# Optimization experiments

Measured on AMD Instinct MI355X. Metric: run time of the kernel, lower is better.

Reference implementation:

```python
import jax, jax.numpy as jnp
import numpy as np

B, T, C, H = 8, 2048, 1024, 128

def setup_inputs() -> dict:
    key = jax.random.key(0)
    kx, kq, kk, kv = jax.random.split(key, 4)
    x = jax.random.normal(kx, (B, T, C), dtype=jnp.float32)
    Wq = jax.random.normal(kq, (C, H), dtype=jnp.float32) * 0.02
    Wk = jax.random.normal(kk, (C, H), dtype=jnp.float32) * 0.02
    Wv = jax.random.normal(kv, (C, H), dtype=jnp.float32) * 0.02
    return {"x": x, "Wq": Wq, "Wk": Wk, "Wv": Wv}

def reference(x, Wq, Wk, Wv):
    # q,k,v: [B,T,H] via bias-free dense projections
    q = jnp.einsum('btc,ch->bth', x, Wq)
    k = jnp.einsum('btc,ch->bth', x, Wk)
    v = jnp.einsum('btc,ch->bth', x, Wv)
    scale = k.shape[-1] ** (-0.5)
    # scores: [B,T,T]
    wei = jnp.einsum('bth,bsh->bts', q, k) * scale
    Tlen = x.shape[1]
    causal = jnp.tril(jnp.ones((Tlen, Tlen), dtype=bool))  # True = keep
    wei = jnp.where(causal[None, :, :], wei, -jnp.inf)
    wei = jax.nn.softmax(wei, axis=-1)
    return jnp.einsum('bts,bsh->bth', wei, v)
```

## Files before the change

kernel.cpp:

```cpp
#include <hip/hip_runtime.h>

#define B_ 8
#define T_ 2048
#define C_ 1024
#define H_ 128
#define BT_ (B_*T_)

typedef unsigned short u16;
typedef unsigned int u32;
typedef __attribute__((ext_vector_type(4))) float f32x4;
typedef __attribute__((ext_vector_type(8))) __bf16 bf16x8;

__device__ __forceinline__ u16 f2bf(float f) {
  u32 u = __float_as_uint(f);
  u += 0x7fffu + ((u >> 16) & 1u);
  return (u16)(u >> 16);
}

#define GLL16(g, l) __builtin_amdgcn_global_load_lds( \
    (const __attribute__((address_space(1))) void*)(g), \
    (__attribute__((address_space(3))) void*)(l), 16, 0, 0)

__device__ __forceinline__ bf16x8 load_frag(const u16* base, int stride, int row0, int k0, int lane) {
  const u16* p = base + (size_t)(row0 + (lane & 15)) * stride + k0 + ((lane >> 4) << 3);
  return *reinterpret_cast<const bf16x8*>(p);
}

__device__ __forceinline__ bf16x8 cvt8(f32x4 lo, f32x4 hi) {
  union { u16 h[8]; bf16x8 v; } u;
#pragma unroll
  for (int i = 0; i < 4; i++) { u.h[i] = f2bf(lo[i]); u.h[4 + i] = f2bf(hi[i]); }
  return u.v;
}

__global__ void wt_kernel(const float* __restrict__ Wq, const float* __restrict__ Wk,
                          const float* __restrict__ Wv, u16* __restrict__ wt) {
  int mat = blockIdx.y;
  const float* W = (mat == 0) ? Wq : (mat == 1) ? Wk : Wv;
  int i = blockIdx.x * 256 + threadIdx.x;
  int h = i >> 10;
  int c = i & 1023;
  wt[mat * (C_ * H_) + i] = f2bf(W[c * H_ + h]);
}

__global__ __launch_bounds__(512) void qkv_gemm(const float* __restrict__ x, const u16* __restrict__ wt,
                                                u16* __restrict__ q, u16* __restrict__ k2,
                                                u16* __restrict__ vt) {
  __shared__ __align__(16) float As[2][64 * 32];
  __shared__ __align__(16) u16 Bs[2][3 * 128 * 32];
  int t = threadIdx.x;
  int lane = t & 63, w = t >> 6;
  int wm = w >> 2, wn = w & 3;
  int quad = lane >> 4, col = lane & 15;
  int m0 = blockIdx.x * 64;

  int arow = t >> 3;
  int agr = (t & 7) ^ (arow & 7);
  const float* axg = x + (size_t)(m0 + arow) * C_ + agr * 4;
  const u16* bwg = wt + (size_t)(t >> 2) * C_ + (t & 3) * 8;

  GLL16(axg, &As[0][w * 256]);
#pragma unroll
  for (int p = 0; p < 3; p++)
    GLL16(bwg + (size_t)p * 128 * C_, &Bs[0][p * 4096 + w * 512]);

  f32x4 acc[2][6] = {};
  for (int kk = 0; kk < 32; kk++) {
    int cur = kk & 1, nxt = cur ^ 1;
    __syncthreads();
    if (kk + 1 < 32) {
      int kn = (kk + 1) * 32;
      GLL16(axg + kn, &As[nxt][w * 256]);
#pragma unroll
      for (int p = 0; p < 3; p++)
        GLL16(bwg + (size_t)p * 128 * C_ + kn, &Bs[nxt][p * 4096 + w * 512]);
    }
    const float* Ab = &As[cur][0];
    const u16* Bb = &Bs[cur][0];
    bf16x8 af[2];
#pragma unroll
    for (int mt = 0; mt < 2; mt++) {
      int r = wm * 32 + mt * 16 + col;
      int s0 = (quad * 2) ^ (r & 7);
      int s1 = (quad * 2 + 1) ^ (r & 7);
      f32x4 lo = *reinterpret_cast<const f32x4*>(Ab + r * 32 + s0 * 4);
      f32x4 hi = *reinterpret_cast<const f32x4*>(Ab + r * 32 + s1 * 4);
      af[mt] = cvt8(lo, hi);
    }
    bf16x8 bfr[6];
#pragma unroll
    for (int nt = 0; nt < 6; nt++) {
      int n = wn * 96 + nt * 16 + col;
      bfr[nt] = *reinterpret_cast<const bf16x8*>(Bb + n * 32 + quad * 8);
    }
#pragma unroll
    for (int mt = 0; mt < 2; mt++)
#pragma unroll
      for (int nt = 0; nt < 6; nt++)
        acc[mt][nt] = __builtin_amdgcn_mfma_f32_16x16x32_bf16(af[mt], bfr[nt], acc[mt][nt], 0, 0, 0);
  }

#pragma unroll
  for (int mt = 0; mt < 2; mt++) {
    int row0 = m0 + wm * 32 + mt * 16 + quad * 4;
#pragma unroll
    for (int nt = 0; nt < 6; nt++) {
      int n = wn * 96 + nt * 16 + col;
      int mat = n >> 7, h = n & 127;
      if (mat == 0) {
#pragma unroll
        for (int r = 0; r < 4; r++) q[(size_t)(row0 + r) * H_ + h] = f2bf(acc[mt][nt][r]);
      } else if (mat == 1) {
#pragma unroll
        for (int r = 0; r < 4; r++) k2[(size_t)(row0 + r) * H_ + h] = f2bf(acc[mt][nt][r]);
      } else {
        int bb = row0 >> 11, tt = row0 & 2047;
        ushort4 pk;
        pk.x = f2bf(acc[mt][nt][0]); pk.y = f2bf(acc[mt][nt][1]);
        pk.z = f2bf(acc[mt][nt][2]); pk.w = f2bf(acc[mt][nt][3]);
        *reinterpret_cast<ushort4*>(&vt[((size_t)bb * H_ + h) * T_ + tt]) = pk;
      }
    }
  }
}

__global__ __launch_bounds__(256) void attn_part(const u16* __restrict__ q, const u16* __restrict__ k,
                                                 const u16* __restrict__ vt,
                                                 float* __restrict__ Op, float* __restrict__ lsum) {
  __shared__ __align__(16) u16 Ks[2][32 * 136];
  __shared__ __align__(16) u16 Vs[2][128 * 40];
  __shared__ __align__(16) u16 P[4][2][16 * 40];
  int t = threadIdx.x;
  int lane = t & 63, w = t >> 6;
  int quad = lane >> 4, col = lane & 15;
  int bx = blockIdx.x;
  int qt = 31 - (bx >> 4);
  int s = (bx >> 3) & 1;
  int b = bx & 7;
  const float scale = 0.08838834764831845f;

  int nk = 2 * (qt + 1);
  int n0 = qt + 1;
  int it0 = s ? n0 : 0;
  int it1 = s ? nk : n0;

  int krow0 = t >> 4, ke = (t & 15) * 8;
  int krow1 = krow0 + 16;
  int vrow0 = t >> 2, ve = (t & 3) * 8;
  int vrow1 = vrow0 + 64;

  int qrow0 = b * T_ + qt * 64 + w * 16;
  bf16x8 qf[4];
#pragma unroll
  for (int ks = 0; ks < 4; ks++) qf[ks] = load_frag(q, H_, qrow0, ks * 32, lane);

  f32x4 o[8] = {};
  float l[4] = {0.f, 0.f, 0.f, 0.f};
  int myqrow = qt * 64 + w * 16 + quad * 4;

  {
    const u16* kb = k + (size_t)(b * T_ + it0 * 32) * H_;
    *reinterpret_cast<uint4*>(&Ks[0][krow0 * 136 + ke]) = *reinterpret_cast<const uint4*>(kb + (size_t)krow0 * 128 + ke);
    *reinterpret_cast<uint4*>(&Ks[0][krow1 * 136 + ke]) = *reinterpret_cast<const uint4*>(kb + (size_t)krow1 * 128 + ke);
    const u16* vb = vt + (size_t)b * H_ * T_ + it0 * 32;
    *reinterpret_cast<uint4*>(&Vs[0][vrow0 * 40 + ve]) = *reinterpret_cast<const uint4*>(vb + (size_t)vrow0 * T_ + ve);
    *reinterpret_cast<uint4*>(&Vs[0][vrow1 * 40 + ve]) = *reinterpret_cast<const uint4*>(vb + (size_t)vrow1 * T_ + ve);
  }

  for (int kt = it0; kt < it1; kt++) {
    int cur = (kt - it0) & 1;
    __syncthreads();
    bool more = (kt + 1 < it1);
    uint4 kc0, kc1, vc0, vc1;
    if (more) {
      const u16* kb = k + (size_t)(b * T_ + (kt + 1) * 32) * H_;
      kc0 = *reinterpret_cast<const uint4*>(kb + (size_t)krow0 * 128 + ke);
      kc1 = *reinterpret_cast<const uint4*>(kb + (size_t)krow1 * 128 + ke);
      const u16* vb = vt + (size_t)b * H_ * T_ + (kt + 1) * 32;
      vc0 = *reinterpret_cast<const uint4*>(vb + (size_t)vrow0 * T_ + ve);
      vc1 = *reinterpret_cast<const uint4*>(vb + (size_t)vrow1 * T_ + ve);
    }

    f32x4 s0 = {}, s1 = {};
#pragma unroll
    for (int ks = 0; ks < 4; ks++) {
      bf16x8 kb0 = *reinterpret_cast<const bf16x8*>(&Ks[cur][col * 136 + ks * 32 + quad * 8]);
      bf16x8 kb1 = *reinterpret_cast<const bf16x8*>(&Ks[cur][(col + 16) * 136 + ks * 32 + quad * 8]);
      s0 = __builtin_amdgcn_mfma_f32_16x16x32_bf16(qf[ks], kb0, s0, 0, 0, 0);
      s1 = __builtin_amdgcn_mfma_f32_16x16x32_bf16(qf[ks], kb1, s1, 0, 0, 0);
    }

    float pv[8];
    int kcol0 = kt * 32 + col;
#pragma unroll
    for (int r = 0; r < 4; r++) {
      int qr = myqrow + r;
      float a0 = fminf(s0[r] * scale, 30.f);
      float a1 = fminf(s1[r] * scale, 30.f);
      a0 = (kcol0      > qr) ? -1e30f : a0;
      a1 = (kcol0 + 16 > qr) ? -1e30f : a1;
      float p0 = __expf(a0);
      float p1 = __expf(a1);
      pv[r] = p0; pv[4 + r] = p1;
      l[r] += p0 + p1;
    }

    u16* Pb = &P[w][cur][0];
#pragma unroll
    for (int r = 0; r < 4; r++) {
      Pb[(quad * 4 + r) * 40 + col] = f2bf(pv[r]);
      Pb[(quad * 4 + r) * 40 + col + 16] = f2bf(pv[4 + r]);
    }
    asm volatile("" ::: "memory");
    __builtin_amdgcn_s_waitcnt(0xc07f);
    asm volatile("" ::: "memory");
    bf16x8 pf = *reinterpret_cast<const bf16x8*>(&Pb[col * 40 + (quad << 3)]);

#pragma unroll
    for (int ht = 0; ht < 8; ht++) {
      bf16x8 vf = *reinterpret_cast<const bf16x8*>(&Vs[cur][(ht * 16 + col) * 40 + quad * 8]);
      o[ht] = __builtin_amdgcn_mfma_f32_16x16x32_bf16(pf, vf, o[ht], 0, 0, 0);
    }

    if (more) {
      int nxt = cur ^ 1;
      *reinterpret_cast<uint4*>(&Ks[nxt][krow0 * 136 + ke]) = kc0;
      *reinterpret_cast<uint4*>(&Ks[nxt][krow1 * 136 + ke]) = kc1;
      *reinterpret_cast<uint4*>(&Vs[nxt][vrow0 * 40 + ve]) = vc0;
      *reinterpret_cast<uint4*>(&Vs[nxt][vrow1 * 40 + ve]) = vc1;
    }
  }

#pragma unroll
  for (int r = 0; r < 4; r++) {
    float v = l[r];
    v += __shfl_xor(v, 1);
    v += __shfl_xor(v, 2);
    v += __shfl_xor(v, 4);
    v += __shfl_xor(v, 8);
    l[r] = v;
  }

  int tile = (s * 8 + b) * 32 + qt;
  float* Orow = Op + (size_t)tile * (64 * 128);
  float* lrow = lsum + (size_t)tile * 64;
  int rowin0 = w * 16 + quad * 4;
  if (col == 0) {
#pragma unroll
    for (int r = 0; r < 4; r++) lrow[rowin0 + r] = l[r];
  }
#pragma unroll
  for (int ht = 0; ht < 8; ht++) {
#pragma unroll
    for (int r = 0; r < 4; r++)
      Orow[(size_t)(rowin0 + r) * 128 + ht * 16 + col] = o[ht][r];
  }
}

__global__ __launch_bounds__(256) void attn_comb(const float* __restrict__ Op, const float* __restrict__ lsum,
                                                 float* __restrict__ out) {
  int bx = blockIdx.x;
  int b = bx >> 5, qt = bx & 31;
  int t = threadIdx.x;
  int h = t & 127, half = t >> 7;
  int tile0 = b * 32 + qt;
  int tile1 = tile0 + 256;
#pragma unroll 4
  for (int rr = 0; rr < 32; rr++) {
    int row = half * 32 + rr;
    float l0 = lsum[tile0 * 64 + row];
    float l1 = lsum[tile1 * 64 + row];
    float rl = 1.f / (l0 + l1);
    float v = (Op[(size_t)tile0 * 8192 + row * 128 + h] +
               Op[(size_t)tile1 * 8192 + row * 128 + h]) * rl;
    out[((size_t)(b * T_ + qt * 64 + row)) * H_ + h] = v;
  }
}

extern "C" void kernel_launch(void* const* d_in, const int* in_sizes, int n_in,
                              void* d_out, int out_size, void* d_ws, size_t ws_size,
                              hipStream_t stream) {
  (void)in_sizes; (void)n_in; (void)out_size; (void)ws_size;
  const float* x  = (const float*)d_in[0];
  const float* Wq = (const float*)d_in[1];
  const float* Wk = (const float*)d_in[2];
  const float* Wv = (const float*)d_in[3];
  u16* ws = (u16*)d_ws;
  u16* q  = ws;
  u16* k  = ws + (size_t)BT_ * H_;
  u16* vt = ws + 2 * (size_t)BT_ * H_;
  u16* wt = ws + 3 * (size_t)BT_ * H_;
  float* Op = (float*)(ws + 3 * (size_t)BT_ * H_ + 3 * C_ * H_);
  float* lsum = Op + (size_t)512 * 64 * 128;
  float* out = (float*)d_out;

  wt_kernel<<<dim3(512, 3), 256, 0, stream>>>(Wq, Wk, Wv, wt);
  qkv_gemm<<<dim3(256), 512, 0, stream>>>(x, wt, q, k, vt);
  attn_part<<<dim3(512), 256, 0, stream>>>(q, k, vt, Op, lsum);
  attn_comb<<<dim3(256), 256, 0, stream>>>(Op, lsum, out);
}
```

Baseline: 180.9 us.

## Split QKV projection GEMM across a grid dimension per weight matrix

The fused QKV GEMM, which computed all three projections per 64-row tile with 512 threads, becomes one block per (row tile, matrix) with 256 threads and a 64x128 output tile. This triples the block count from 256 to 768 so all compute units have work, and shrinks shared memory per block. In exchange, each x tile is loaded from global memory and converted to bf16 three times instead of once.

```diff
diff --git a/kernel.cpp b/kernel.cpp
--- a/kernel.cpp
+++ b/kernel.cpp
@@ -43,37 +43,41 @@
   wt[mat * (C_ * H_) + i] = f2bf(W[c * H_ + h]);
 }
 
-__global__ __launch_bounds__(512) void qkv_gemm(const float* __restrict__ x, const u16* __restrict__ wt,
+__global__ __launch_bounds__(256) void qkv_gemm(const float* __restrict__ x, const u16* __restrict__ wt,
                                                 u16* __restrict__ q, u16* __restrict__ k2,
                                                 u16* __restrict__ vt) {
   __shared__ __align__(16) float As[2][64 * 32];
-  __shared__ __align__(16) u16 Bs[2][3 * 128 * 32];
+  __shared__ __align__(16) u16 Bs[2][128 * 32];
   int t = threadIdx.x;
   int lane = t & 63, w = t >> 6;
-  int wm = w >> 2, wn = w & 3;
+  int wm = w >> 1, wn = w & 1;
   int quad = lane >> 4, col = lane & 15;
   int m0 = blockIdx.x * 64;
-
-  int arow = t >> 3;
-  int agr = (t & 7) ^ (arow & 7);
-  const float* axg = x + (size_t)(m0 + arow) * C_ + agr * 4;
-  const u16* bwg = wt + (size_t)(t >> 2) * C_ + (t & 3) * 8;
-
-  GLL16(axg, &As[0][w * 256]);
-#pragma unroll
-  for (int p = 0; p < 3; p++)
-    GLL16(bwg + (size_t)p * 128 * C_, &Bs[0][p * 4096 + w * 512]);
-
-  f32x4 acc[2][6] = {};
+  int mat = blockIdx.y;
+  const u16* wmp = wt + (size_t)mat * (C_ * H_);
+
+  int ar0 = t >> 3, ar1 = ar0 + 32;
+  const float* ax0 = x + (size_t)(m0 + ar0) * C_ + (((t & 7) ^ (ar0 & 7)) << 2);
+  const float* ax1 = x + (size_t)(m0 + ar1) * C_ + (((t & 7) ^ (ar1 & 7)) << 2);
+  const u16* bw0 = wmp + (size_t)(t >> 2) * C_ + ((t & 3) << 3);
+  const u16* bw1 = bw0 + (size_t)64 * C_;
+
+  GLL16(ax0, &As[0][w * 256]);
+  GLL16(ax1, &As[0][w * 256 + 1024]);
+  GLL16(bw0, &Bs[0][w * 512]);
+  GLL16(bw1, &Bs[0][2048 + w * 512]);
+
+  f32x4 acc[2][4] = {};
   for (int kk = 0; kk < 32; kk++) {
-    int cur = kk & 1, nxt = cur ^ 1;
+    int cur = kk & 1;
     __syncthreads();
     if (kk + 1 < 32) {
+      int nxt = cur ^ 1;
       int kn = (kk + 1) * 32;
-      GLL16(axg + kn, &As[nxt][w * 256]);
-#pragma unroll
-      for (int p = 0; p < 3; p++)
-        GLL16(bwg + (size_t)p * 128 * C_ + kn, &Bs[nxt][p * 4096 + w * 512]);
+      GLL16(ax0 + kn, &As[nxt][w * 256]);
+      GLL16(ax1 + kn, &As[nxt][w * 256 + 1024]);
+      GLL16(bw0 + kn, &Bs[nxt][w * 512]);
+      GLL16(bw1 + kn, &Bs[nxt][2048 + w * 512]);
     }
     const float* Ab = &As[cur][0];
     const u16* Bb = &Bs[cur][0];
@@ -82,21 +86,21 @@
     for (int mt = 0; mt < 2; mt++) {
       int r = wm * 32 + mt * 16 + col;
       int s0 = (quad * 2) ^ (r & 7);
-      int s1 = (quad * 2 + 1) ^ (r & 7);
+      int s1 = s0 ^ 1;
       f32x4 lo = *reinterpret_cast<const f32x4*>(Ab + r * 32 + s0 * 4);
       f32x4 hi = *reinterpret_cast<const f32x4*>(Ab + r * 32 + s1 * 4);
       af[mt] = cvt8(lo, hi);
     }
-    bf16x8 bfr[6];
-#pragma unroll
-    for (int nt = 0; nt < 6; nt++) {
-      int n = wn * 96 + nt * 16 + col;
+    bf16x8 bfr[4];
+#pragma unroll
+    for (int nt = 0; nt < 4; nt++) {
+      int n = wn * 64 + nt * 16 + col;
       bfr[nt] = *reinterpret_cast<const bf16x8*>(Bb + n * 32 + quad * 8);
     }
 #pragma unroll
     for (int mt = 0; mt < 2; mt++)
 #pragma unroll
-      for (int nt = 0; nt < 6; nt++)
+      for (int nt = 0; nt < 4; nt++)
         acc[mt][nt] = __builtin_amdgcn_mfma_f32_16x16x32_bf16(af[mt], bfr[nt], acc[mt][nt], 0, 0, 0);
   }
 
@@ -104,21 +108,20 @@
   for (int mt = 0; mt < 2; mt++) {
     int row0 = m0 + wm * 32 + mt * 16 + quad * 4;
 #pragma unroll
-    for (int nt = 0; nt < 6; nt++) {
-      int n = wn * 96 + nt * 16 + col;
-      int mat = n >> 7, h = n & 127;
+    for (int nt = 0; nt < 4; nt++) {
+      int n = wn * 64 + nt * 16 + col;
       if (mat == 0) {
 #pragma unroll
-        for (int r = 0; r < 4; r++) q[(size_t)(row0 + r) * H_ + h] = f2bf(acc[mt][nt][r]);
+        for (int r = 0; r < 4; r++) q[(size_t)(row0 + r) * H_ + n] = f2bf(acc[mt][nt][r]);
       } else if (mat == 1) {
 #pragma unroll
-        for (int r = 0; r < 4; r++) k2[(size_t)(row0 + r) * H_ + h] = f2bf(acc[mt][nt][r]);
+        for (int r = 0; r < 4; r++) k2[(size_t)(row0 + r) * H_ + n] = f2bf(acc[mt][nt][r]);
       } else {
         int bb = row0 >> 11, tt = row0 & 2047;
         ushort4 pk;
         pk.x = f2bf(acc[mt][nt][0]); pk.y = f2bf(acc[mt][nt][1]);
         pk.z = f2bf(acc[mt][nt][2]); pk.w = f2bf(acc[mt][nt][3]);
-        *reinterpret_cast<ushort4*>(&vt[((size_t)bb * H_ + h) * T_ + tt]) = pk;
+        *reinterpret_cast<ushort4*>(&vt[((size_t)bb * H_ + n) * T_ + tt]) = pk;
       }
     }
   }
@@ -295,7 +298,7 @@
   float* out = (float*)d_out;
 
   wt_kernel<<<dim3(512, 3), 256, 0, stream>>>(Wq, Wk, Wv, wt);
-  qkv_gemm<<<dim3(256), 512, 0, stream>>>(x, wt, q, k, vt);
+  qkv_gemm<<<dim3(BT_ / 64, 3), 256, 0, stream>>>(x, wt, q, k, vt);
   attn_part<<<dim3(512), 256, 0, stream>>>(q, k, vt, Op, lsum);
   attn_comb<<<dim3(256), 256, 0, stream>>>(Op, lsum, out);
 }
```

Measured after the change: 175.6 us. -2.9%, faster.

## Load QKV GEMM operands directly from global memory, dropping LDS staging

Applied to the files above, without the earlier changes.

The QKV projection GEMM stops staging x and weight tiles through double-buffered LDS with global_load_lds and barriers. Each wave now reads its MFMA fragments straight from global memory, with native bf16 casts and a 2x unrolled k-loop, and launch bounds ask for two blocks per CU. This removes LDS traffic and per-iteration __syncthreads. In exchange, fragment loads are strided per lane (each lane reads its own row), and x is re-read by all four column waves, leaning on cache instead of LDS reuse.

```diff
diff --git a/kernel.cpp b/kernel.cpp
--- a/kernel.cpp
+++ b/kernel.cpp
@@ -17,20 +17,16 @@
   return (u16)(u >> 16);
 }
 
-#define GLL16(g, l) __builtin_amdgcn_global_load_lds( \
-    (const __attribute__((address_space(1))) void*)(g), \
-    (__attribute__((address_space(3))) void*)(l), 16, 0, 0)
-
 __device__ __forceinline__ bf16x8 load_frag(const u16* base, int stride, int row0, int k0, int lane) {
   const u16* p = base + (size_t)(row0 + (lane & 15)) * stride + k0 + ((lane >> 4) << 3);
   return *reinterpret_cast<const bf16x8*>(p);
 }
 
-__device__ __forceinline__ bf16x8 cvt8(f32x4 lo, f32x4 hi) {
-  union { u16 h[8]; bf16x8 v; } u;
-#pragma unroll
-  for (int i = 0; i < 4; i++) { u.h[i] = f2bf(lo[i]); u.h[4 + i] = f2bf(hi[i]); }
-  return u.v;
+__device__ __forceinline__ bf16x8 cvt8n(f32x4 lo, f32x4 hi) {
+  bf16x8 r;
+#pragma unroll
+  for (int i = 0; i < 4; i++) { r[i] = (__bf16)lo[i]; r[4 + i] = (__bf16)hi[i]; }
+  return r;
 }
 
 __global__ void wt_kernel(const float* __restrict__ Wq, const float* __restrict__ Wk,
@@ -43,56 +39,35 @@
   wt[mat * (C_ * H_) + i] = f2bf(W[c * H_ + h]);
 }
 
-__global__ __launch_bounds__(512) void qkv_gemm(const float* __restrict__ x, const u16* __restrict__ wt,
-                                                u16* __restrict__ q, u16* __restrict__ k2,
-                                                u16* __restrict__ vt) {
-  __shared__ __align__(16) float As[2][64 * 32];
-  __shared__ __align__(16) u16 Bs[2][3 * 128 * 32];
+__global__ __launch_bounds__(512, 2) void qkv_gemm(const float* __restrict__ x, const u16* __restrict__ wt,
+                                                   u16* __restrict__ q, u16* __restrict__ k2,
+                                                   u16* __restrict__ vt) {
   int t = threadIdx.x;
   int lane = t & 63, w = t >> 6;
   int wm = w >> 2, wn = w & 3;
   int quad = lane >> 4, col = lane & 15;
   int m0 = blockIdx.x * 64;
 
-  int arow = t >> 3;
-  int agr = (t & 7) ^ (arow & 7);
-  const float* axg = x + (size_t)(m0 + arow) * C_ + agr * 4;
-  const u16* bwg = wt + (size_t)(t >> 2) * C_ + (t & 3) * 8;
-
-  GLL16(axg, &As[0][w * 256]);
-#pragma unroll
-  for (int p = 0; p < 3; p++)
-    GLL16(bwg + (size_t)p * 128 * C_, &Bs[0][p * 4096 + w * 512]);
+  const float* a0 = x + (size_t)(m0 + wm * 32 + col) * C_ + quad * 8;
+  const float* a1 = a0 + (size_t)16 * C_;
+  const u16* b0 = wt + (size_t)(wn * 96 + col) * C_ + quad * 8;
 
   f32x4 acc[2][6] = {};
+#pragma unroll 2
   for (int kk = 0; kk < 32; kk++) {
-    int cur = kk & 1, nxt = cur ^ 1;
-    __syncthreads();
-    if (kk + 1 < 32) {
-      int kn = (kk + 1) * 32;
-      GLL16(axg + kn, &As[nxt][w * 256]);
-#pragma unroll
-      for (int p = 0; p < 3; p++)
-        GLL16(bwg + (size_t)p * 128 * C_ + kn, &Bs[nxt][p * 4096 + w * 512]);
-    }
-    const float* Ab = &As[cur][0];
-    const u16* Bb = &Bs[cur][0];
-    bf16x8 af[2];
-#pragma unroll
-    for (int mt = 0; mt < 2; mt++) {
-      int r = wm * 32 + mt * 16 + col;
-      int s0 = (quad * 2) ^ (r & 7);
-      int s1 = (quad * 2 + 1) ^ (r & 7);
-      f32x4 lo = *reinterpret_cast<const f32x4*>(Ab + r * 32 + s0 * 4);
-      f32x4 hi = *reinterpret_cast<const f32x4*>(Ab + r * 32 + s1 * 4);
-      af[mt] = cvt8(lo, hi);
-    }
-    bf16x8 bfr[6];
-#pragma unroll
-    for (int nt = 0; nt < 6; nt++) {
-      int n = wn * 96 + nt * 16 + col;
-      bfr[nt] = *reinterpret_cast<const bf16x8*>(Bb + n * 32 + quad * 8);
-    }
+    int k0 = kk * 32;
+    bf16x8 af[2], bfr[6];
+    {
+      f32x4 lo0 = *reinterpret_cast<const f32x4*>(a0 + k0);
+      f32x4 hi0 = *reinterpret_cast<const f32x4*>(a0 + k0 + 4);
+      f32x4 lo1 = *reinterpret_cast<const f32x4*>(a1 + k0);
+      f32x4 hi1 = *reinterpret_cast<const f32x4*>(a1 + k0 + 4);
+      af[0] = cvt8n(lo0, hi0);
+      af[1] = cvt8n(lo1, hi1);
+    }
+#pragma unroll
+    for (int nt = 0; nt < 6; nt++)
+      bfr[nt] = *reinterpret_cast<const bf16x8*>(b0 + (size_t)nt * 16 * C_ + k0);
 #pragma unroll
     for (int mt = 0; mt < 2; mt++)
 #pragma unroll
@@ -295,7 +270,7 @@
   float* out = (float*)d_out;
 
   wt_kernel<<<dim3(512, 3), 256, 0, stream>>>(Wq, Wk, Wv, wt);
-  qkv_gemm<<<dim3(256), 512, 0, stream>>>(x, wt, q, k, vt);
+  qkv_gemm<<<dim3(BT_ / 64), 512, 0, stream>>>(x, wt, q, k, vt);
   attn_part<<<dim3(512), 256, 0, stream>>>(q, k, vt, Op, lsum);
   attn_comb<<<dim3(256), 256, 0, stream>>>(Op, lsum, out);
 }
```

Result: slower. 210.4 us (+16.3%).
